# Kernel optimization log

Hardware: AMD Instinct MI355X
Metric: run time of the kernel (lower is better)

Reference implementation:

```python
import jax, jax.numpy as jnp
import numpy as np

B, S, D_MODEL, H, D_HEAD = 4, 2048, 512, 8, 64

def setup_inputs() -> dict:
    key = jax.random.key(0)
    ks = jax.random.split(key, 11)
    scale = 0.02
    inp = {
        "Q": jax.random.normal(ks[0], (B, S, D_MODEL), dtype=jnp.float32),
        "K": jax.random.normal(ks[1], (B, S, D_MODEL), dtype=jnp.float32),
        "V": jax.random.normal(ks[2], (B, S, D_MODEL), dtype=jnp.float32),
        # Linear weights stored as [in, out] so y = x @ W + b
        "Wq": jax.random.normal(ks[3], (D_MODEL, H * D_HEAD), dtype=jnp.float32) * scale,
        "bq": jnp.zeros((H * D_HEAD,), dtype=jnp.float32),
        "Wk": jax.random.normal(ks[4], (D_MODEL, H * D_HEAD), dtype=jnp.float32) * scale,
        "bk": jnp.zeros((H * D_HEAD,), dtype=jnp.float32),
        "Wv": jax.random.normal(ks[5], (D_MODEL, H * D_HEAD), dtype=jnp.float32) * scale,
        "bv": jnp.zeros((H * D_HEAD,), dtype=jnp.float32),
        "Wo": jax.random.normal(ks[6], (D_MODEL, D_MODEL), dtype=jnp.float32) * scale,
        "bo": jnp.zeros((D_MODEL,), dtype=jnp.float32),
    }
    return inp


def reference(Q, K, V, Wq, bq, Wk, bk, Wv, bv, Wo, bo):
    b = Q.shape[0]
    # project and split heads: [B, S, H*d] -> [B, H, S, d]
    def split_heads(x):
        return x.reshape(b, -1, H, D_HEAD).transpose(0, 2, 1, 3)
    q = split_heads(Q @ Wq + bq)
    k = split_heads(K @ Wk + bk)
    v = split_heads(V @ Wv + bv)
    # naive attention with materialized [B, H, S, S] scores (mask=False path)
    scores = jnp.einsum("bhqd,bhkd->bhqk", q, k) / jnp.sqrt(jnp.float32(D_HEAD))
    probs = jax.nn.softmax(scores, axis=-1)
    z = jnp.einsum("bhqk,bhkd->bhqd", probs, v)
    # merge heads: [B, H, S, d] -> [B, S, H*d]
    z = z.transpose(0, 2, 1, 3).reshape(b, -1, H * D_HEAD)
    return z @ Wo + bo
```

## Files before the change

kernel.cpp:

```cpp
#include <hip/hip_runtime.h>


typedef unsigned short u16;
typedef __bf16 bf16x8 __attribute__((ext_vector_type(8)));
typedef float  f32x4  __attribute__((ext_vector_type(4)));

__device__ __forceinline__ u16 f2bf(float x) {
  unsigned u = __float_as_uint(x);
  u += 0x7fffu + ((u >> 16) & 1u);
  return (u16)(u >> 16);
}

__device__ __forceinline__ unsigned cvtpk(float lo, float hi) {
  unsigned r;
  asm("v_cvt_pk_bf16_f32 %0, %1, %2" : "=v"(r) : "v"(lo), "v"(hi));
  return r;
}

__device__ __forceinline__ f32x4 mfma16(bf16x8 a, bf16x8 b, f32x4 c) {
  return __builtin_amdgcn_mfma_f32_16x16x32_bf16(a, b, c, 0, 0, 0);
}

__device__ __forceinline__ void gl16(const u16* g, u16* l) {
  __builtin_amdgcn_global_load_lds(
      (const __attribute__((address_space(1))) void*)g,
      (__attribute__((address_space(3))) void*)l, 16, 0, 0);
}

#define MX3(a, b, c) fmaxf(fmaxf((a), (b)), (c))

__global__ __launch_bounds__(256) void prep_k(const float* __restrict__ W0,
                                              const float* __restrict__ W1,
                                              const float* __restrict__ W2,
                                              const float* __restrict__ W3,
                                              u16* __restrict__ Wt,
                                              const float* __restrict__ Q,
                                              const float* __restrict__ K,
                                              const float* __restrict__ V,
                                              u16* __restrict__ Oq,
                                              u16* __restrict__ Ok,
                                              u16* __restrict__ Ov) {
  int y = blockIdx.y;
  if (y < 4) {
    if (blockIdx.x >= 1024) return;
    const float* W = y == 0 ? W0 : y == 1 ? W1 : y == 2 ? W2 : W3;
    int idx = blockIdx.x * 256 + threadIdx.x;
    int k = idx >> 9, n = idx & 511;
    Wt[y * 262144 + n * 512 + k] = f2bf(W[idx]);
  } else {
    int sel = y - 4;
    const float* X = sel == 0 ? Q : sel == 1 ? K : V;
    u16* O = sel == 0 ? Oq : sel == 1 ? Ok : Ov;
    size_t i = ((size_t)blockIdx.x * 256 + threadIdx.x) * 8;
    float4 a = *(const float4*)(X + i);
    float4 b = *(const float4*)(X + i + 4);
    uint4 pk = make_uint4(cvtpk(a.x, a.y), cvtpk(a.z, a.w),
                          cvtpk(b.x, b.y), cvtpk(b.z, b.w));
    *(uint4*)(O + i) = pk;
  }
}

template <int OUT_MODE, int BN>
__device__ __forceinline__ void gemm_body(const u16* __restrict__ A,
                                          const u16* __restrict__ Bt,
                                          const float* __restrict__ bias,
                                          void* __restrict__ outp, int bidx) {
  constexpr int NF = BN / 32;
  constexpr int NBN = 512 / BN;
  __shared__ __align__(16) u16 As[128][64];
  __shared__ __align__(16) u16 Bs[BN][64];
  int tid = threadIdx.x;
  int lane = tid & 63, wid = tid >> 6;
  int wm = wid >> 1, wn = wid & 1;
  int lr = lane & 15, lg = lane >> 4;
  int bm = bidx / NBN, bn = bidx % NBN;

  int r0 = tid >> 3;
  int c8s = (tid & 7) ^ (r0 & 7);
  const u16* Ab = A + (size_t)(bm * 128) * 512;
  const u16* Bb = Bt + (size_t)(bn * BN) * 512;

  f32x4 acc[4][NF];
#pragma unroll
  for (int i = 0; i < 4; ++i)
#pragma unroll
    for (int j = 0; j < NF; ++j) {
      f32x4 z = {0.f, 0.f, 0.f, 0.f};
      acc[i][j] = z;
    }

#pragma unroll
  for (int kt = 0; kt < 8; ++kt) {
    int k0 = kt * 64;
#pragma unroll
    for (int i = 0; i < 4; ++i)
      gl16(&Ab[(size_t)(i * 32 + r0) * 512 + k0 + c8s * 8],
           &As[0][0] + i * 2048 + wid * 512);
#pragma unroll
    for (int i = 0; i < BN / 32; ++i)
      gl16(&Bb[(size_t)(i * 32 + r0) * 512 + k0 + c8s * 8],
           &Bs[0][0] + i * 2048 + wid * 512);
    __syncthreads();
#pragma unroll
    for (int kk = 0; kk < 2; ++kk) {
      bf16x8 af[4], bfr[NF];
      int sw = (lr & 7) << 3;
#pragma unroll
      for (int mf = 0; mf < 4; ++mf)
        af[mf] = *(const bf16x8*)&As[wm * 64 + mf * 16 + lr][(kk * 32 + lg * 8) ^ sw];
#pragma unroll
      for (int nf = 0; nf < NF; ++nf)
        bfr[nf] = *(const bf16x8*)&Bs[wn * (BN / 2) + nf * 16 + lr][(kk * 32 + lg * 8) ^ sw];
#pragma unroll
      for (int mf = 0; mf < 4; ++mf)
#pragma unroll
        for (int nf = 0; nf < NF; ++nf)
          acc[mf][nf] = mfma16(af[mf], bfr[nf], acc[mf][nf]);
    }
    __syncthreads();
  }

#pragma unroll
  for (int mf = 0; mf < 4; ++mf) {
#pragma unroll
    for (int nf = 0; nf < NF; ++nf) {
      int m = bm * 128 + wm * 64 + mf * 16 + lg * 4;
      int n = bn * BN + wn * (BN / 2) + nf * 16 + lr;
      float bia = bias[n];
      if (OUT_MODE == 0) {
        u16* o = (u16*)outp;
#pragma unroll
        for (int r = 0; r < 4; ++r)
          o[(size_t)(m + r) * 512 + n] = f2bf(acc[mf][nf][r] + bia);
      } else if (OUT_MODE == 2) {
        float* o = (float*)outp;
#pragma unroll
        for (int r = 0; r < 4; ++r)
          o[(size_t)(m + r) * 512 + n] = acc[mf][nf][r] + bia;
      } else {
        u16* o = (u16*)outp;
        int b = m >> 11, s = m & 2047;
        int h = n >> 6, d = n & 63;
        ushort4 pk = make_ushort4(f2bf(acc[mf][nf][0] + bia), f2bf(acc[mf][nf][1] + bia),
                                  f2bf(acc[mf][nf][2] + bia), f2bf(acc[mf][nf][3] + bia));
        *(ushort4*)&o[(size_t)((b * 8 + h) * 64 + d) * 2048 + s] = pk;
      }
    }
  }
}

__global__ __launch_bounds__(256) void qkv_k(const u16* __restrict__ Aq,
                                             const u16* __restrict__ Ak,
                                             const u16* __restrict__ Av,
                                             const u16* __restrict__ Wt,
                                             const float* __restrict__ bq,
                                             const float* __restrict__ bk,
                                             const float* __restrict__ bv,
                                             u16* __restrict__ outbase) {
  int sel = blockIdx.y;
  const u16* A = sel == 0 ? Aq : sel == 1 ? Ak : Av;
  const float* bia = sel == 0 ? bq : sel == 1 ? bk : bv;
  const u16* Bt = Wt + (size_t)sel * 262144;
  u16* out = outbase + (size_t)sel * 8192 * 512;
  if (sel == 2)
    gemm_body<1, 128>(A, Bt, bia, out, blockIdx.x);
  else
    gemm_body<0, 128>(A, Bt, bia, out, blockIdx.x);
}

__global__ __launch_bounds__(256) void gemm_out_k(const u16* __restrict__ Ap,
                                                  const u16* __restrict__ Bt,
                                                  const float* __restrict__ bias,
                                                  void* __restrict__ outp) {
  gemm_body<2, 64>(Ap, Bt, bias, outp, blockIdx.x);
}

__global__ __launch_bounds__(256) void attn_k(const u16* __restrict__ q,
                                              const u16* __restrict__ kmat,
                                              const u16* __restrict__ vT,
                                              u16* __restrict__ z) {
  __shared__ __align__(16) u16 Ks[2][64][64];
  __shared__ __align__(16) u16 Vs[64][64];
  __shared__ __align__(16) u16 Ps[4][16][72];
  const float C = 0.125f * 1.44269504f;
  int tid = threadIdx.x;
  int lane = tid & 63, w = tid >> 6;
  int lr = lane & 15, lg = lane >> 4;
  int bh = blockIdx.x >> 5, qt = blockIdx.x & 31;
  int b = bh >> 3, h = bh & 7;
  size_t qrow0 = (size_t)(b * 2048 + qt * 64 + w * 16);

  bf16x8 qf[2];
#pragma unroll
  for (int kf = 0; kf < 2; ++kf)
    qf[kf] = *(const bf16x8*)&q[(qrow0 + lr) * 512 + h * 64 + kf * 32 + lg * 8];

  f32x4 oacc[4];
#pragma unroll
  for (int j = 0; j < 4; ++j) {
    f32x4 zf = {0.f, 0.f, 0.f, 0.f};
    oacc[j] = zf;
  }
  float m = -1e30f, l_part = 0.f, negmC = 0.f;

  const u16* kbase = kmat + (size_t)(b * 2048) * 512 + h * 64;
  const u16* vbase = vT + (size_t)(bh * 64) * 2048;

  int r0 = tid >> 3;
  int c8s = (tid & 7) ^ (r0 & 7);
  int sw = (lr & 7) << 3;
  gl16(&kbase[(size_t)r0 * 512 + c8s * 8],        &Ks[0][0][0] + w * 512);
  gl16(&kbase[(size_t)(r0 + 32) * 512 + c8s * 8], &Ks[0][0][0] + 2048 + w * 512);
  __syncthreads();

  auto tile = [&](int kt, const u16* Kc, u16* Kn) {
    gl16(&vbase[(size_t)r0 * 2048 + kt * 64 + c8s * 8],        &Vs[0][0] + w * 512);
    gl16(&vbase[(size_t)(r0 + 32) * 2048 + kt * 64 + c8s * 8], &Vs[0][0] + 2048 + w * 512);
    if (kt < 31) {
      gl16(&kbase[(size_t)((kt + 1) * 64 + r0) * 512 + c8s * 8],       Kn + w * 512);
      gl16(&kbase[(size_t)((kt + 1) * 64 + r0 + 32) * 512 + c8s * 8],  Kn + 2048 + w * 512);
    }

    f32x4 sacc[4];
#pragma unroll
    for (int j = 0; j < 4; ++j) {
      f32x4 zf = {0.f, 0.f, 0.f, 0.f};
      sacc[j] = zf;
    }
#pragma unroll
    for (int kf = 0; kf < 2; ++kf) {
#pragma unroll
      for (int nf = 0; nf < 4; ++nf) {
        int row = nf * 16 + lr;
        bf16x8 kb = *(const bf16x8*)&Kc[row * 64 + ((kf * 32 + lg * 8) ^ sw)];
        sacc[nf] = mfma16(kb, qf[kf], sacc[nf]);
      }
    }

    float t0 = MX3(sacc[0][0], sacc[0][1], sacc[0][2]);
    float t1 = MX3(sacc[0][3], sacc[1][0], sacc[1][1]);
    float t2 = MX3(sacc[1][2], sacc[1][3], sacc[2][0]);
    float t3 = MX3(sacc[2][1], sacc[2][2], sacc[2][3]);
    float t4 = MX3(sacc[3][0], sacc[3][1], sacc[3][2]);
    float mxl = fmaxf(MX3(t0, t1, t2), MX3(t3, t4, sacc[3][3]));

    if (!__all(mxl - m <= 8.f)) {
      float mx = fmaxf(mxl, __shfl_xor(mxl, 16));
      mx = fmaxf(mx, __shfl_xor(mx, 32));
      float mnew = fmaxf(m, mx);
      float sc = __builtin_amdgcn_exp2f((m - mnew) * C);
      m = mnew;
      negmC = -m * C;
      l_part *= sc;
#pragma unroll
      for (int nfo = 0; nfo < 4; ++nfo)
#pragma unroll
        for (int r = 0; r < 4; ++r) oacc[nfo][r] *= sc;
    }

    float rsum = 0.f;
#pragma unroll
    for (int nf = 0; nf < 4; ++nf) {
      float p0 = __builtin_amdgcn_exp2f(fmaf(sacc[nf][0], C, negmC));
      float p1 = __builtin_amdgcn_exp2f(fmaf(sacc[nf][1], C, negmC));
      float p2 = __builtin_amdgcn_exp2f(fmaf(sacc[nf][2], C, negmC));
      float p3 = __builtin_amdgcn_exp2f(fmaf(sacc[nf][3], C, negmC));
      rsum += (p0 + p1) + (p2 + p3);
      uint2 pw = make_uint2(cvtpk(p0, p1), cvtpk(p2, p3));
      *(uint2*)&Ps[w][lr][nf * 16 + lg * 4] = pw;
    }
    l_part += rsum;

    asm volatile("s_waitcnt lgkmcnt(0)" ::: "memory");
    if (kt < 31) {
      asm volatile("s_waitcnt vmcnt(2)" ::: "memory");
    } else {
      asm volatile("s_waitcnt vmcnt(0)" ::: "memory");
    }
    __builtin_amdgcn_s_barrier();

#pragma unroll
    for (int ks = 0; ks < 2; ++ks) {
      bf16x8 pa = *(const bf16x8*)&Ps[w][lr][ks * 32 + lg * 8];
#pragma unroll
      for (int nfo = 0; nfo < 4; ++nfo) {
        int row = nfo * 16 + lr;
        bf16x8 vbr = *(const bf16x8*)&Vs[row][(ks * 32 + lg * 8) ^ sw];
        oacc[nfo] = mfma16(vbr, pa, oacc[nfo]);
      }
    }
    __syncthreads();
  };

  for (int ko = 0; ko < 32; ko += 2) {
    tile(ko,     &Ks[0][0][0], &Ks[1][0][0]);
    tile(ko + 1, &Ks[1][0][0], &Ks[0][0][0]);
  }

  float l = l_part + __shfl_xor(l_part, 16);
  l += __shfl_xor(l, 32);
  float rl = 1.f / l;
#pragma unroll
  for (int nfo = 0; nfo < 4; ++nfo) {
    uint2 pw = make_uint2(cvtpk(oacc[nfo][0] * rl, oacc[nfo][1] * rl),
                          cvtpk(oacc[nfo][2] * rl, oacc[nfo][3] * rl));
    *(uint2*)&z[(qrow0 + lr) * 512 + h * 64 + nfo * 16 + lg * 4] = pw;
  }
}

extern "C" void kernel_launch(void* const* d_in, const int* in_sizes, int n_in,
                              void* d_out, int out_size, void* d_ws, size_t ws_size,
                              hipStream_t stream) {
  const float* Q  = (const float*)d_in[0];
  const float* K  = (const float*)d_in[1];
  const float* V  = (const float*)d_in[2];
  const float* Wq = (const float*)d_in[3];
  const float* bq = (const float*)d_in[4];
  const float* Wk = (const float*)d_in[5];
  const float* bk = (const float*)d_in[6];
  const float* Wv = (const float*)d_in[7];
  const float* bv = (const float*)d_in[8];
  const float* Wo = (const float*)d_in[9];
  const float* bo = (const float*)d_in[10];
  float* out = (float*)d_out;

  u16* ws  = (u16*)d_ws;
  u16* Wt  = ws;
  u16* qws = Wt + 4 * 262144;
  u16* kws = qws + (size_t)8192 * 512;
  u16* vTw = kws + (size_t)8192 * 512;
  u16* zws = vTw + (size_t)8192 * 512;

  u16* AbfQ = (u16*)d_out;
  u16* AbfK = AbfQ + (size_t)8192 * 512;
  u16* AbfV = zws;

  prep_k<<<dim3(2048, 7), 256, 0, stream>>>(Wq, Wk, Wv, Wo, Wt, Q, K, V,
                                            AbfQ, AbfK, AbfV);
  qkv_k<<<dim3(256, 3), 256, 0, stream>>>(AbfQ, AbfK, AbfV, Wt, bq, bk, bv, qws);
  attn_k<<<1024, 256, 0, stream>>>(qws, kws, vTw, zws);
  gemm_out_k<<<512, 256, 0, stream>>>(zws, Wt + 3 * 262144, bo, out);
}
```

Baseline: 119.1 us.

## Load V fragments directly into registers with double-buffered prefetch instead of LDS

The attention kernel stops staging the transposed V tile through shared memory. Each lane now loads its MFMA B-operand fragments of V straight from global memory into registers, one tile ahead, alternating between two register sets. The mid-tile barrier that waited for the V copy into LDS is removed, leaving only a sched_barrier. This cuts LDS traffic and a synchronization point, at the cost of 64 extra VGPRs for the double buffer, possible occupancy loss, and uncoalesced 16-byte global reads strided by 2048 elements.

After: 218.6 us. 83.6% more time.

```diff
diff --git a/kernel.cpp b/kernel.cpp
--- a/kernel.cpp
+++ b/kernel.cpp
@@ -180,7 +180,6 @@
                                               const u16* __restrict__ vT,
                                               u16* __restrict__ z) {
   __shared__ __align__(16) u16 Ks[2][64][64];
-  __shared__ __align__(16) u16 Vs[64][64];
   __shared__ __align__(16) u16 Ps[4][16][72];
   const float C = 0.125f * 1.44269504f;
   int tid = threadIdx.x;
@@ -205,20 +204,35 @@
 
   const u16* kbase = kmat + (size_t)(b * 2048) * 512 + h * 64;
   const u16* vbase = vT + (size_t)(bh * 64) * 2048;
+  const u16* vfrag = vbase + (size_t)lr * 2048 + lg * 8;
 
   int r0 = tid >> 3;
   int c8s = (tid & 7) ^ (r0 & 7);
   int sw = (lr & 7) << 3;
+
+  bf16x8 vb0[2][4], vb1[2][4];
+
   gl16(&kbase[(size_t)r0 * 512 + c8s * 8],        &Ks[0][0][0] + w * 512);
   gl16(&kbase[(size_t)(r0 + 32) * 512 + c8s * 8], &Ks[0][0][0] + 2048 + w * 512);
+#pragma unroll
+  for (int ks = 0; ks < 2; ++ks)
+#pragma unroll
+    for (int nfo = 0; nfo < 4; ++nfo)
+      vb0[ks][nfo] = *(const bf16x8*)&vfrag[(size_t)(nfo * 16) * 2048 + ks * 32];
+  asm volatile("s_waitcnt vmcnt(0)" ::: "memory");
   __syncthreads();
 
-  auto tile = [&](int kt, const u16* Kc, u16* Kn) {
-    gl16(&vbase[(size_t)r0 * 2048 + kt * 64 + c8s * 8],        &Vs[0][0] + w * 512);
-    gl16(&vbase[(size_t)(r0 + 32) * 2048 + kt * 64 + c8s * 8], &Vs[0][0] + 2048 + w * 512);
+  auto tile = [&](int kt, const u16* Kc, u16* Kn,
+                  bf16x8 (&vbu)[2][4], bf16x8 (&vbl)[2][4]) {
     if (kt < 31) {
-      gl16(&kbase[(size_t)((kt + 1) * 64 + r0) * 512 + c8s * 8],       Kn + w * 512);
-      gl16(&kbase[(size_t)((kt + 1) * 64 + r0 + 32) * 512 + c8s * 8],  Kn + 2048 + w * 512);
+      gl16(&kbase[(size_t)((kt + 1) * 64 + r0) * 512 + c8s * 8],      Kn + w * 512);
+      gl16(&kbase[(size_t)((kt + 1) * 64 + r0 + 32) * 512 + c8s * 8], Kn + 2048 + w * 512);
+      const u16* vf = vfrag + (kt + 1) * 64;
+#pragma unroll
+      for (int ks = 0; ks < 2; ++ks)
+#pragma unroll
+        for (int nfo = 0; nfo < 4; ++nfo)
+          vbl[ks][nfo] = *(const bf16x8*)&vf[(size_t)(nfo * 16) * 2048 + ks * 32];
     }
 
     f32x4 sacc[4];
@@ -272,29 +286,23 @@
     l_part += rsum;
 
     asm volatile("s_waitcnt lgkmcnt(0)" ::: "memory");
-    if (kt < 31) {
-      asm volatile("s_waitcnt vmcnt(2)" ::: "memory");
-    } else {
-      asm volatile("s_waitcnt vmcnt(0)" ::: "memory");
-    }
-    __builtin_amdgcn_s_barrier();
+    __builtin_amdgcn_sched_barrier(0);
 
 #pragma unroll
     for (int ks = 0; ks < 2; ++ks) {
       bf16x8 pa = *(const bf16x8*)&Ps[w][lr][ks * 32 + lg * 8];
 #pragma unroll
-      for (int nfo = 0; nfo < 4; ++nfo) {
-        int row = nfo * 16 + lr;
-        bf16x8 vbr = *(const bf16x8*)&Vs[row][(ks * 32 + lg * 8) ^ sw];
-        oacc[nfo] = mfma16(vbr, pa, oacc[nfo]);
-      }
-    }
+      for (int nfo = 0; nfo < 4; ++nfo)
+        oacc[nfo] = mfma16(vbu[ks][nfo], pa, oacc[nfo]);
+    }
+
+    asm volatile("s_waitcnt vmcnt(0)" ::: "memory");
     __syncthreads();
   };
 
   for (int ko = 0; ko < 32; ko += 2) {
-    tile(ko,     &Ks[0][0][0], &Ks[1][0][0]);
-    tile(ko + 1, &Ks[1][0][0], &Ks[0][0][0]);
+    tile(ko,     &Ks[0][0][0], &Ks[1][0][0], vb0, vb1);
+    tile(ko + 1, &Ks[1][0][0], &Ks[0][0][0], vb1, vb0);
   }
 
   float l = l_part + __shfl_xor(l_part, 16);
```
